# Optimization experiments

Hardware: AMD Instinct MI355X
Metric: run time of the kernel (lower is better)

Reference implementation:

```python
import jax, jax.numpy as jnp
import numpy as np

B, N = 32, 8192
NUM_CLASSES = 40
SA1_DIMS = (3, 64, 64, 128)      # grouped relative xyz only (in_channels=3 -> no extra features)
SA2_DIMS = (131, 128, 128, 256)  # 128 SA1 features + 3 relative xyz
LOC_DIMS = (256, 256, 512, 1024)
GLOB_DIMS = (1024, 512, 256)


def _fps(xyz, m):
    """Farthest point sampling. xyz: [B,N,3] -> indices [B,m] (first index is point 0)."""
    b, n, _ = xyz.shape
    big = jnp.asarray(1e10, xyz.dtype)

    def step(carry, _):
        dists, last = carry                                   # [B,N], [B]
        p = jnp.take_along_axis(xyz, last[:, None, None], axis=1)  # [B,1,3]
        d = jnp.sum((xyz - p) ** 2, axis=-1)                  # [B,N]
        dists = jnp.minimum(dists, d)
        nxt = jnp.argmax(dists, axis=-1).astype(jnp.int32)
        return (dists, nxt), nxt

    init = (jnp.full((b, n), big, xyz.dtype), jnp.zeros((b,), jnp.int32))
    _, rest = jax.lax.scan(step, init, None, length=m - 1)    # [m-1,B]
    return jnp.concatenate([jnp.zeros((b, 1), jnp.int32), rest.T], axis=1)


def _ball_query(xyz, new_xyz, radius, k):
    """First-k points within radius of each centroid, padded with the first hit (CUDA ball_query semantics)."""
    d2 = jnp.sum((new_xyz[:, :, None, :] - xyz[:, None, :, :]) ** 2, axis=-1)  # [B,M,N]
    valid = d2 < radius * radius
    n = xyz.shape[1]
    ar = jnp.arange(n, dtype=jnp.int32)
    order_key = jnp.where(valid, ar, ar + n)                  # valid points sort first, in index order
    _, idx = jax.lax.top_k(-order_key, k)                     # [B,M,K] first-k valid indices
    num_valid = jnp.sum(valid, axis=-1)                       # [B,M]
    idx = jnp.where(jnp.arange(k) < num_valid[..., None], idx, idx[..., :1])
    return idx.astype(jnp.int32)


_gather = jax.vmap(lambda p, i: p[i])  # p:[N,C], i:[M,K] -> [M,K,C], vmapped over batch


def _sa(xyz, feats, m, radius, k, ws, bs):
    """PointNetSAModule: FPS -> ball query -> group (relative xyz [+feat]) -> SharedMLP -> max over K."""
    cidx = _fps(xyz, m)
    new_xyz = jnp.take_along_axis(xyz, cidx[:, :, None], axis=1)   # [B,m,3]
    idx = _ball_query(xyz, new_xyz, radius, k)                     # [B,m,k]
    x = _gather(xyz, idx) - new_xyz[:, :, None, :]                 # [B,m,k,3]
    if feats is not None:
        x = jnp.concatenate([x, _gather(feats, idx)], axis=-1)
    for w, b in zip(ws, bs):  # Conv2d(1x1)+BN(eval, folded)+ReLU
        x = jax.nn.relu(jnp.einsum('bmkc,oc->bmko', x, w) + b)
    return new_xyz, jnp.max(x, axis=2)                             # [B,m,C_out]


def _forward(points, sa1_w0, sa1_b0, sa1_w1, sa1_b1, sa1_w2, sa1_b2,
             sa2_w0, sa2_b0, sa2_w1, sa2_b1, sa2_w2, sa2_b2,
             loc_w0, loc_b0, loc_w1, loc_b1, loc_w2, loc_b2,
             glob_w0, glob_b0, glob_w1, glob_b1, cls_w, cls_b):
    xyz = jnp.transpose(points, (0, 2, 1))                         # [B,N,3]
    new_xyz, feats = _sa(xyz, None, 512, 0.2, 32,
                         (sa1_w0, sa1_w1, sa1_w2), (sa1_b0, sa1_b1, sa1_b2))
    _, feats = _sa(new_xyz, feats, 128, 0.4, 64,
                   (sa2_w0, sa2_w1, sa2_w2), (sa2_b0, sa2_b1, sa2_b2))
    x = feats                                                      # [B,128,256]
    for w, b in ((loc_w0, loc_b0), (loc_w1, loc_b1), (loc_w2, loc_b2)):
        x = jax.nn.relu(jnp.einsum('bnc,oc->bno', x, w) + b)       # SharedMLP (Conv1d+BN+ReLU)
    x = jnp.max(x, axis=1)                                         # global max-pool -> [B,1024]
    for w, b in ((glob_w0, glob_b0), (glob_w1, glob_b1)):          # MLP (dropout in eval = identity)
        x = jax.nn.relu(x @ w.T + b)
    return x @ cls_w.T + cls_b                                     # cls_logits [B,40]


def setup_inputs() -> dict:
    key = jax.random.key(0)
    ks = iter(jax.random.split(key, 64))
    inp = {}
    # unit-cube point cloud so radii 0.2/0.4 are geometrically meaningful
    inp['points'] = jax.random.uniform(next(ks), (B, 3, N), jnp.float32, -1.0, 1.0)

    def lin(co, ci):
        return jax.random.normal(next(ks), (co, ci), jnp.float32) / np.sqrt(ci)

    for name, dims in (('sa1', SA1_DIMS), ('sa2', SA2_DIMS), ('loc', LOC_DIMS)):
        for i in range(len(dims) - 1):
            inp[f'{name}_w{i}'] = lin(dims[i + 1], dims[i])
            inp[f'{name}_b{i}'] = 0.01 * jax.random.normal(next(ks), (dims[i + 1],), jnp.float32)
    for i in range(2):
        inp[f'glob_w{i}'] = lin(GLOB_DIMS[i + 1], GLOB_DIMS[i])
        inp[f'glob_b{i}'] = 0.01 * jax.random.normal(next(ks), (GLOB_DIMS[i + 1],), jnp.float32)
    inp['cls_w'] = lin(NUM_CLASSES, GLOB_DIMS[-1])
    inp['cls_b'] = jnp.zeros((NUM_CLASSES,), jnp.float32)
    return inp


def reference(points, sa1_w0, sa1_b0, sa1_w1, sa1_b1, sa1_w2, sa1_b2,
              sa2_w0, sa2_b0, sa2_w1, sa2_b1, sa2_w2, sa2_b2,
              loc_w0, loc_b0, loc_w1, loc_b1, loc_w2, loc_b2,
              glob_w0, glob_b0, glob_w1, glob_b1, cls_w, cls_b):
    return _forward(points, sa1_w0, sa1_b0, sa1_w1, sa1_b1, sa1_w2, sa1_b2,
                    sa2_w0, sa2_b0, sa2_w1, sa2_b1, sa2_w2, sa2_b2,
                    loc_w0, loc_b0, loc_w1, loc_b1, loc_w2, loc_b2,
                    glob_w0, glob_b0, glob_w1, glob_b1, cls_w, cls_b)
```

## Files before the change

kernel.cpp:

```cpp
#include <hip/hip_runtime.h>
#include <hip/hip_bf16.h>
#include <cstdint>

#define CDIV(a,b) (((a)+(b)-1)/(b))

typedef short s8v __attribute__((ext_vector_type(8)));
typedef float f4v __attribute__((ext_vector_type(4)));
typedef float f2v __attribute__((ext_vector_type(2)));

__device__ __forceinline__ unsigned short f2bf_bits(float v) {
  __hip_bfloat16 b = __float2bfloat16(v);
  unsigned short u; __builtin_memcpy(&u, &b, 2);
  return u;
}
__device__ __forceinline__ void bsplit(float v, unsigned short& h, unsigned short& l) {
  __hip_bfloat16 hb = __float2bfloat16(v);
  float hf = __bfloat162float(hb);
  unsigned short hu; __builtin_memcpy(&hu, &hb, 2);
  h = hu;
  l = f2bf_bits(v - hf);
}

__device__ __forceinline__ void agpr_put(float& slot, float v) {
  asm volatile("v_accvgpr_write_b32 %0, %1" : "=a"(slot) : "v"(v));
}
__device__ __forceinline__ float agpr_get(const float& slot) {
  float v;
  asm volatile("v_accvgpr_read_b32 %0, %1" : "=v"(v) : "a"(slot));
  return v;
}

__device__ __forceinline__ f2v pk_add(f2v a, f2v b) {
  f2v d; asm("v_pk_add_f32 %0, %1, %2" : "=v"(d) : "v"(a), "v"(b)); return d;
}
__device__ __forceinline__ f2v pk_mul(f2v a, f2v b) {
  f2v d; asm("v_pk_mul_f32 %0, %1, %2" : "=v"(d) : "v"(a), "v"(b)); return d;
}
__device__ __forceinline__ f2v pk_fma(f2v a, f2v b, f2v c) {
  f2v d; asm("v_pk_fma_f32 %0, %1, %2, %3" : "=v"(d) : "v"(a), "v"(b), "v"(c)); return d;
}

template<int C>
__device__ __forceinline__ unsigned dpp32(unsigned v) {
  return (unsigned)__builtin_amdgcn_update_dpp((int)v, (int)v, C, 0xF, 0xF, false);
}
template<int C>
__device__ __forceinline__ unsigned long long red_key(unsigned long long pk) {
  unsigned lo = dpp32<C>((unsigned)pk);
  unsigned hi = dpp32<C>((unsigned)(pk >> 32));
  unsigned long long p2 = ((unsigned long long)hi << 32) | lo;
  return (p2 > pk) ? p2 : pk;
}

template<int NPTS, int MOUT, int NTHR>
__global__ __launch_bounds__(NTHR, 1) void fps_kernel(
    const float* __restrict__ pts, int bstride, int cstride,
    float* __restrict__ aos, float* __restrict__ soa)
{
  constexpr int PPT = NPTS / NTHR;
  constexpr int NP2 = PPT / 2;
  constexpr int NW  = NTHR / 64;
  const int b = blockIdx.x, t = threadIdx.x;
  const int lane = t & 63;
  const int wid = t >> 6;
  const float* px = pts + (size_t)b * bstride;
  const float* py = px + cstride;
  const float* pz = px + 2 * cstride;
  __shared__ float s_x[NPTS], s_y[NPTS], s_z[NPTS];
  __shared__ unsigned long long s_key[2][NW > 1 ? NW : 1];
  __shared__ int s_out[MOUT];

  float ax[PPT], ay[PPT], az[PPT];
  f2v dsv[NP2];
#pragma unroll
  for (int j = 0; j < PPT; ++j) {
    int i = t + j * NTHR;
    float x = px[i], y = py[i], z = pz[i];
    s_x[i] = x; s_y[i] = y; s_z[i] = z;
    agpr_put(ax[j], x); agpr_put(ay[j], y); agpr_put(az[j], z);
  }
#pragma unroll
  for (int q = 0; q < NP2; ++q) dsv[q] = (f2v){1e10f, 1e10f};
  if (t == 0) s_out[0] = 0;
  float lx = px[0], ly = py[0], lz = pz[0];
  __syncthreads();

  for (int it = 1; it < MOUT; ++it) {
    const f2v nlx = (f2v){-lx, -lx};
    const f2v nly = (f2v){-ly, -ly};
    const f2v nlz = (f2v){-lz, -lz};
    float bestv = -1.0f; int bestj = 0;
#pragma unroll
    for (int q = 0; q < NP2; ++q) {
      f2v x2, y2, z2;
      x2.x = agpr_get(ax[2 * q]); x2.y = agpr_get(ax[2 * q + 1]);
      y2.x = agpr_get(ay[2 * q]); y2.y = agpr_get(ay[2 * q + 1]);
      z2.x = agpr_get(az[2 * q]); z2.y = agpr_get(az[2 * q + 1]);
      f2v dx = pk_add(x2, nlx);
      f2v dy = pk_add(y2, nly);
      f2v dz = pk_add(z2, nlz);
      f2v d2 = pk_fma(dz, dz, pk_fma(dy, dy, pk_mul(dx, dx)));
      float nd0 = fminf(dsv[q].x, d2.x);
      float nd1 = fminf(dsv[q].y, d2.y);
      dsv[q].x = nd0; dsv[q].y = nd1;
      if (nd0 > bestv) { bestv = nd0; bestj = 2 * q; }
      if (nd1 > bestv) { bestv = nd1; bestj = 2 * q + 1; }
    }
    const int besti = t + bestj * NTHR;
    unsigned long long pk =
        ((unsigned long long)__float_as_uint(bestv) << 32) | (unsigned)(~(unsigned)besti);
    pk = red_key<0x111>(pk);
    pk = red_key<0x112>(pk);
    pk = red_key<0x114>(pk);
    pk = red_key<0x118>(pk);
    pk = red_key<0x142>(pk);
    pk = red_key<0x143>(pk);
    int widx;
    if constexpr (NW == 1) {
      widx = (int)(~(unsigned)__builtin_amdgcn_readlane((int)(unsigned)pk, 63));
    } else {
      const int pb = it & 1;
      if (lane == 63) s_key[pb][wid] = pk;
      __syncthreads();
      unsigned long long ck = s_key[pb][lane & (NW - 1)];
      if (NW >= 2)  ck = red_key<0x111>(ck);
      if (NW >= 4)  ck = red_key<0x112>(ck);
      if (NW >= 8)  ck = red_key<0x114>(ck);
      if (NW >= 16) ck = red_key<0x118>(ck);
      widx = (int)(~(unsigned)__builtin_amdgcn_readlane((int)(unsigned)ck, NW - 1));
    }
    lx = s_x[widx]; ly = s_y[widx]; lz = s_z[widx];
    if (t == 0) s_out[it] = widx;
  }
  __syncthreads();
  for (int i = t; i < MOUT; i += NTHR) {
    const int idx = s_out[i];
    const float x = s_x[idx], y = s_y[idx], z = s_z[idx];
    float* a = aos + ((size_t)b * MOUT + i) * 3;
    a[0] = x; a[1] = y; a[2] = z;
    soa[(size_t)b * 3 * MOUT + i]            = x;
    soa[(size_t)b * 3 * MOUT + MOUT + i]     = y;
    soa[(size_t)b * 3 * MOUT + 2 * MOUT + i] = z;
  }
}

template<int NPTS, int KNB, int MC>
__global__ __launch_bounds__(64) void ballq_wave(
    const float* __restrict__ pts, int bstride, int cstride,
    const float* __restrict__ cents, int* __restrict__ out, float r2)
{
  constexpr int NCH = NPTS / 128;
  const int g = blockIdx.x;
  const int b = g / MC;
  const int lane = threadIdx.x;
  const float* px = pts + (size_t)b * bstride;
  const float* py = px + cstride;
  const float* pz = px + 2 * cstride;
  const float cx = cents[g * 3 + 0], cy = cents[g * 3 + 1], cz = cents[g * 3 + 2];
  __shared__ int s_idx[KNB];
  float ax0 = px[lane],      ay0 = py[lane],      az0 = pz[lane];
  float ax1 = px[64 + lane], ay1 = py[64 + lane], az1 = pz[64 + lane];
  int base = 0;
  const unsigned long long below = (1ull << lane) - 1ull;
  for (int c = 0; c < NCH; ++c) {
    float X0 = ax0, Y0 = ay0, Z0 = az0;
    float X1 = ax1, Y1 = ay1, Z1 = az1;
    if (c + 1 < NCH) {
      int i0 = (c + 1) * 128 + lane;
      ax0 = px[i0];      ay0 = py[i0];      az0 = pz[i0];
      ax1 = px[i0 + 64]; ay1 = py[i0 + 64]; az1 = pz[i0 + 64];
    }
    float dx0 = X0 - cx, dy0 = Y0 - cy, dz0 = Z0 - cz;
    float dx1 = X1 - cx, dy1 = Y1 - cy, dz1 = Z1 - cz;
    bool v0 = (dx0 * dx0 + dy0 * dy0 + dz0 * dz0) < r2;
    bool v1 = (dx1 * dx1 + dy1 * dy1 + dz1 * dz1) < r2;
    unsigned long long m0 = __ballot(v0);
    unsigned long long m1 = __ballot(v1);
    int r0 = __popcll(m0 & below);
    int p0 = base + r0;
    if (v0 && p0 < KNB) s_idx[p0] = c * 128 + lane;
    int base1 = base + __popcll(m0);
    int r1 = __popcll(m1 & below);
    int p1 = base1 + r1;
    if (v1 && p1 < KNB) s_idx[p1] = c * 128 + 64 + lane;
    base = base1 + __popcll(m1);
    if (base >= KNB) break;
  }
  int total = base < KNB ? base : KNB;
  int first = s_idx[0];
  if (lane < KNB)
    out[(size_t)g * KNB + lane] = (lane < total) ? s_idx[lane] : first;
}

__device__ void fps2_embed(
    const float* __restrict__ soa_in, int b,
    float* __restrict__ aos, float* __restrict__ soa,
    float* fx, float* fy, float* fz, int* fout,
    unsigned long long* fkey , int t)
{
  const int lane = t & 63, wid = t >> 6;
  const float* px = soa_in + (size_t)b * 1536;
  const float* py = px + 512;
  const float* pz = px + 1024;
  float x0, y0, z0, x1, y1, z1;
  {
    const int i0 = t, i1 = t + 256;
    x0 = px[i0]; y0 = py[i0]; z0 = pz[i0];
    x1 = px[i1]; y1 = py[i1]; z1 = pz[i1];
    fx[i0] = x0; fy[i0] = y0; fz[i0] = z0;
    fx[i1] = x1; fy[i1] = y1; fz[i1] = z1;
  }
  f2v ds = (f2v){1e10f, 1e10f};
  if (t == 0) fout[0] = 0;
  float lx = px[0], ly = py[0], lz = pz[0];
  __syncthreads();
  for (int it = 1; it < 128; ++it) {
    f2v X = (f2v){x0, x1}, Y = (f2v){y0, y1}, Z = (f2v){z0, z1};
    f2v dx = pk_add(X, (f2v){-lx, -lx});
    f2v dy = pk_add(Y, (f2v){-ly, -ly});
    f2v dz = pk_add(Z, (f2v){-lz, -lz});
    f2v d2 = pk_fma(dz, dz, pk_fma(dy, dy, pk_mul(dx, dx)));
    float nd0 = fminf(ds.x, d2.x);
    float nd1 = fminf(ds.y, d2.y);
    ds.x = nd0; ds.y = nd1;
    float bestv = nd0; int bestj = 0;
    if (nd1 > bestv) { bestv = nd1; bestj = 1; }
    const int besti = t + bestj * 256;
    unsigned long long pk =
        ((unsigned long long)__float_as_uint(bestv) << 32) | (unsigned)(~(unsigned)besti);
    pk = red_key<0x111>(pk);
    pk = red_key<0x112>(pk);
    pk = red_key<0x114>(pk);
    pk = red_key<0x118>(pk);
    pk = red_key<0x142>(pk);
    pk = red_key<0x143>(pk);
    const int pb = it & 1;
    if (lane == 63) fkey[pb * 4 + wid] = pk;
    __syncthreads();
    unsigned long long ck = fkey[pb * 4 + (lane & 3)];
    ck = red_key<0x111>(ck);
    ck = red_key<0x112>(ck);
    const int widx = (int)(~(unsigned)__builtin_amdgcn_readlane((int)(unsigned)ck, 3));
    lx = fx[widx]; ly = fy[widx]; lz = fz[widx];
    if (t == 0) fout[it] = widx;
  }
  __syncthreads();
  if (t < 128) {
    const int idx = fout[t];
    const float x = fx[idx], y = fy[idx], z = fz[idx];
    float* a = aos + ((size_t)b * 128 + t) * 3;
    a[0] = x; a[1] = y; a[2] = z;
    soa[(size_t)b * 384 + t]       = x;
    soa[(size_t)b * 384 + 128 + t] = y;
    soa[(size_t)b * 384 + 256 + t] = z;
  }
}

__global__ __launch_bounds__(256, 1) void sa1_fused(
    const float* __restrict__ pts, const int* __restrict__ idx1,
    const float* __restrict__ cents,
    const float* __restrict__ w0, const float* __restrict__ b0,
    const unsigned short* __restrict__ w1h, const unsigned short* __restrict__ w1l,
    const float* __restrict__ b1,
    const unsigned short* __restrict__ w2h, const unsigned short* __restrict__ w2l,
    const float* __restrict__ b2,
    unsigned short* __restrict__ f1h, unsigned short* __restrict__ f1l,
    const float* __restrict__ nx1_soa, float* __restrict__ nx2_aos,
    float* __restrict__ nx2_soa)
{
  __shared__ __align__(16) unsigned short sY[2][128 * 72];
  __shared__ __align__(16) unsigned short sZ[2][128 * 72];
  __shared__ __align__(16) unsigned short sW[2][64 * 72];
  __shared__ float sw0[192];
  __shared__ float sb0[64];

  const int tid = threadIdx.x, lane = tid & 63, wid = tid >> 6;
  const int wm = wid & 1, wn = wid >> 1;
  const int mn15 = lane & 15, kgrp = lane >> 4;

  if (blockIdx.x < 32) {
    float* fx = (float*)&sY[0][0];
    float* fy = fx + 512;
    float* fz = fy + 512;
    int*   fout = (int*)(fz + 512);
    unsigned long long* fkey = (unsigned long long*)(fout + 128);
    fps2_embed(nx1_soa, blockIdx.x, nx2_aos, nx2_soa, fx, fy, fz, fout, fkey, tid);
    return;
  }
  const int bk = blockIdx.x - 32;

  if (tid < 192) sw0[tid] = w0[tid];
  else sb0[tid - 192] = b0[tid - 192];
  for (int gi = tid; gi < 1024; gi += 256) {
    const int pl = gi >> 9, idx = gi & 511;
    const int n = idx >> 3, k8 = idx & 7;
    const uint4 v = ((const uint4*)(pl ? w1l : w1h))[idx];
    *(uint4*)&sW[pl][n * 72 + k8 * 8] = v;
  }
  __syncthreads();

  {
    const int rl = tid >> 1, half = tid & 1;
    const int r = bk * 128 + rl;
    const int gl = r >> 5, j = r & 31, b = gl >> 9;
    const int i = idx1[(size_t)gl * 32 + j];
    const float* px = pts + (size_t)b * 24576;
    const float x = px[i]         - cents[gl * 3 + 0];
    const float y = px[8192 + i]  - cents[gl * 3 + 1];
    const float z = px[16384 + i] - cents[gl * 3 + 2];
    union { unsigned short us[32]; uint4 v[4]; } ph, pl4;
#pragma unroll
    for (int u = 0; u < 32; ++u) {
      const int o = half * 32 + u;
      float v = sw0[o * 3] * x + sw0[o * 3 + 1] * y + sw0[o * 3 + 2] * z + sb0[o];
      v = fmaxf(v, 0.f);
      bsplit(v, ph.us[u], pl4.us[u]);
    }
    const int base = rl * 72 + half * 32;
#pragma unroll
    for (int g = 0; g < 4; ++g) {
      *(uint4*)&sY[0][base + g * 8] = ph.v[g];
      *(uint4*)&sY[1][base + g * 8] = pl4.v[g];
    }
  }
  __syncthreads();

  {
    f4v acc[4][2];
#pragma unroll
    for (int a = 0; a < 4; ++a)
#pragma unroll
      for (int c = 0; c < 2; ++c) acc[a][c] = (f4v){0.f, 0.f, 0.f, 0.f};
#pragma unroll
    for (int kc = 0; kc < 2; ++kc) {
      const int k0 = kc * 32;
      s8v af[2][4], bf[2][2];
#pragma unroll
      for (int mt = 0; mt < 4; ++mt) {
        const int m = wm * 64 + mt * 16 + mn15;
        af[0][mt] = *(const s8v*)&sY[0][m * 72 + k0 + kgrp * 8];
        af[1][mt] = *(const s8v*)&sY[1][m * 72 + k0 + kgrp * 8];
      }
#pragma unroll
      for (int nt = 0; nt < 2; ++nt) {
        const int n = wn * 32 + nt * 16 + mn15;
        bf[0][nt] = *(const s8v*)&sW[0][n * 72 + k0 + kgrp * 8];
        bf[1][nt] = *(const s8v*)&sW[1][n * 72 + k0 + kgrp * 8];
      }
#pragma unroll
      for (int mt = 0; mt < 4; ++mt)
#pragma unroll
        for (int nt = 0; nt < 2; ++nt) {
          acc[mt][nt] = __builtin_amdgcn_mfma_f32_16x16x32_bf16(af[0][mt], bf[0][nt], acc[mt][nt], 0, 0, 0);
          acc[mt][nt] = __builtin_amdgcn_mfma_f32_16x16x32_bf16(af[0][mt], bf[1][nt], acc[mt][nt], 0, 0, 0);
          acc[mt][nt] = __builtin_amdgcn_mfma_f32_16x16x32_bf16(af[1][mt], bf[0][nt], acc[mt][nt], 0, 0, 0);
        }
    }
#pragma unroll
    for (int nt = 0; nt < 2; ++nt) {
      const int n = wn * 32 + nt * 16 + mn15;
      const float bv = b1[n];
#pragma unroll
      for (int mt = 0; mt < 4; ++mt)
#pragma unroll
        for (int r = 0; r < 4; ++r) {
          const int m = wm * 64 + mt * 16 + (lane >> 4) * 4 + r;
          float v = fmaxf(acc[mt][nt][r] + bv, 0.f);
          unsigned short h, l; bsplit(v, h, l);
          sZ[0][m * 72 + n] = h;
          sZ[1][m * 72 + n] = l;
        }
    }
  }
  __syncthreads();

  for (int gi = tid; gi < 2048; gi += 256) {
    const int pl = gi >> 10, idx = gi & 1023;
    const int n = idx >> 3, k8 = idx & 7;
    const uint4 v = ((const uint4*)(pl ? w2l : w2h))[idx];
    *(uint4*)&sY[pl][n * 72 + k8 * 8] = v;
  }
  __syncthreads();

  {
    f4v acc[4][4];
#pragma unroll
    for (int a = 0; a < 4; ++a)
#pragma unroll
      for (int c = 0; c < 4; ++c) acc[a][c] = (f4v){0.f, 0.f, 0.f, 0.f};
#pragma unroll
    for (int kc = 0; kc < 2; ++kc) {
      const int k0 = kc * 32;
      s8v af[2][4], bf[2][4];
#pragma unroll
      for (int mt = 0; mt < 4; ++mt) {
        const int m = wm * 64 + mt * 16 + mn15;
        af[0][mt] = *(const s8v*)&sZ[0][m * 72 + k0 + kgrp * 8];
        af[1][mt] = *(const s8v*)&sZ[1][m * 72 + k0 + kgrp * 8];
      }
#pragma unroll
      for (int nt = 0; nt < 4; ++nt) {
        const int n = wn * 64 + nt * 16 + mn15;
        bf[0][nt] = *(const s8v*)&sY[0][n * 72 + k0 + kgrp * 8];
        bf[1][nt] = *(const s8v*)&sY[1][n * 72 + k0 + kgrp * 8];
      }
#pragma unroll
      for (int mt = 0; mt < 4; ++mt)
#pragma unroll
        for (int nt = 0; nt < 4; ++nt) {
          acc[mt][nt] = __builtin_amdgcn_mfma_f32_16x16x32_bf16(af[0][mt], bf[0][nt], acc[mt][nt], 0, 0, 0);
          acc[mt][nt] = __builtin_amdgcn_mfma_f32_16x16x32_bf16(af[0][mt], bf[1][nt], acc[mt][nt], 0, 0, 0);
          acc[mt][nt] = __builtin_amdgcn_mfma_f32_16x16x32_bf16(af[1][mt], bf[0][nt], acc[mt][nt], 0, 0, 0);
        }
    }
#pragma unroll
    for (int gq = 0; gq < 2; ++gq)
#pragma unroll
      for (int nt = 0; nt < 4; ++nt) {
        const int n = wn * 64 + nt * 16 + mn15;
        float v = -1e30f;
#pragma unroll
        for (int mt = 2 * gq; mt < 2 * gq + 2; ++mt)
#pragma unroll
          for (int r = 0; r < 4; ++r) v = fmaxf(v, acc[mt][nt][r]);
        v = fmaxf(v + b2[n], 0.f);
        v = fmaxf(v, __shfl_xor(v, 16, 64));
        v = fmaxf(v, __shfl_xor(v, 32, 64));
        if (lane < 16) {
          const size_t row = (size_t)bk * 4 + wm * 2 + gq;
          unsigned short h, l; bsplit(v, h, l);
          f1h[row * 128 + n] = h;
          f1l[row * 128 + n] = l;
        }
      }
  }
}

__global__ __launch_bounds__(256, 1) void sa2_fused(
    const unsigned short* __restrict__ f1h, const unsigned short* __restrict__ f1l,
    const float* __restrict__ nx1_aos, const float* __restrict__ nx2_aos,
    const int* __restrict__ idx2,
    const unsigned short* __restrict__ w1h, const unsigned short* __restrict__ w1l,
    const float* __restrict__ b1,
    const unsigned short* __restrict__ w2h, const unsigned short* __restrict__ w2l,
    const float* __restrict__ b2,
    const unsigned short* __restrict__ w3h, const unsigned short* __restrict__ w3l,
    const float* __restrict__ b3,
    unsigned short* __restrict__ f2h, unsigned short* __restrict__ f2l)
{
  __shared__ __align__(16) unsigned short sX[2][64 * 160];
  __shared__ __align__(16) unsigned short sY[2][64 * 136];
  __shared__ __align__(16) unsigned short sW[4][2][32 * 40];

  const int tid = threadIdx.x, lane = tid & 63, wid = tid >> 6;
  const int mn15 = lane & 15, kgrp = lane >> 4;
  const int gg = blockIdx.x;
  const int bb = gg >> 7;

  {
    const int r = tid >> 2, q = tid & 3;
    const int i = idx2[(size_t)gg * 64 + r];
    const int p = bb * 512 + i;
#pragma unroll
    for (int pl = 0; pl < 2; ++pl) {
      const uint4* src = (const uint4*)((pl ? f1l : f1h) + (size_t)p * 128);
#pragma unroll
      for (int g = 0; g < 4; ++g)
        *(uint4*)&sX[pl][r * 160 + (q * 4 + g) * 8] = src[q * 4 + g];
    }
    if (q == 0) {
      union { unsigned short us[8]; uint4 v; } ph, pl4;
#pragma unroll
      for (int u = 0; u < 8; ++u) { ph.us[u] = 0; pl4.us[u] = 0; }
#pragma unroll
      for (int c = 0; c < 3; ++c) {
        float v = nx1_aos[(size_t)p * 3 + c] - nx2_aos[(size_t)gg * 3 + c];
        bsplit(v, ph.us[c], pl4.us[c]);
      }
      *(uint4*)&sX[0][r * 160 + 128] = ph.v;
      *(uint4*)&sX[1][r * 160 + 128] = pl4.v;
    } else {
      uint4 z = make_uint4(0, 0, 0, 0);
      *(uint4*)&sX[0][r * 160 + 128 + q * 8] = z;
      *(uint4*)&sX[1][r * 160 + 128 + q * 8] = z;
    }
  }
  __syncthreads();

  const int spl = lane >> 5, srow = lane & 31;
  unsigned short* swb = &sW[wid][0][0];

  {
    f4v acc[4][2];
#pragma unroll
    for (int a = 0; a < 4; ++a)
#pragma unroll
      for (int c = 0; c < 2; ++c) acc[a][c] = (f4v){0.f, 0.f, 0.f, 0.f};
    uint4 pf[4];
    {
      const unsigned short* s = (spl ? w1l : w1h) + (size_t)(wid * 32 + srow) * 160;
#pragma unroll
      for (int g = 0; g < 4; ++g) pf[g] = *(const uint4*)(s + g * 8);
    }
#pragma unroll
    for (int c = 0; c < 5; ++c) {
      unsigned short* d = swb + spl * 1280 + srow * 40;
#pragma unroll
      for (int g = 0; g < 4; ++g) *(uint4*)(d + g * 8) = pf[g];
      if (c < 4) {
        const unsigned short* s = (spl ? w1l : w1h) + (size_t)(wid * 32 + srow) * 160 + (c + 1) * 32;
#pragma unroll
        for (int g = 0; g < 4; ++g) pf[g] = *(const uint4*)(s + g * 8);
      }
      const int k0 = c * 32;
      s8v af[2][4], bf[2][2];
#pragma unroll
      for (int mt = 0; mt < 4; ++mt) {
        const int m = mt * 16 + mn15;
        af[0][mt] = *(const s8v*)&sX[0][m * 160 + k0 + kgrp * 8];
        af[1][mt] = *(const s8v*)&sX[1][m * 160 + k0 + kgrp * 8];
      }
#pragma unroll
      for (int nt = 0; nt < 2; ++nt) {
        const int nl = nt * 16 + mn15;
        bf[0][nt] = *(const s8v*)&swb[0 * 1280 + nl * 40 + kgrp * 8];
        bf[1][nt] = *(const s8v*)&swb[1 * 1280 + nl * 40 + kgrp * 8];
      }
#pragma unroll
      for (int mt = 0; mt < 4; ++mt)
#pragma unroll
        for (int nt = 0; nt < 2; ++nt) {
          acc[mt][nt] = __builtin_amdgcn_mfma_f32_16x16x32_bf16(af[0][mt], bf[0][nt], acc[mt][nt], 0, 0, 0);
          acc[mt][nt] = __builtin_amdgcn_mfma_f32_16x16x32_bf16(af[0][mt], bf[1][nt], acc[mt][nt], 0, 0, 0);
          acc[mt][nt] = __builtin_amdgcn_mfma_f32_16x16x32_bf16(af[1][mt], bf[0][nt], acc[mt][nt], 0, 0, 0);
        }
    }
#pragma unroll
    for (int nt = 0; nt < 2; ++nt) {
      const int n = wid * 32 + nt * 16 + mn15;
      const float bv = b1[n];
#pragma unroll
      for (int mt = 0; mt < 4; ++mt)
#pragma unroll
        for (int r = 0; r < 4; ++r) {
          const int m = mt * 16 + kgrp * 4 + r;
          float v = fmaxf(acc[mt][nt][r] + bv, 0.f);
          unsigned short h, l; bsplit(v, h, l);
          sY[0][m * 136 + n] = h;
          sY[1][m * 136 + n] = l;
        }
    }
  }
  __syncthreads();

  {
    f4v acc[4][2];
#pragma unroll
    for (int a = 0; a < 4; ++a)
#pragma unroll
      for (int c = 0; c < 2; ++c) acc[a][c] = (f4v){0.f, 0.f, 0.f, 0.f};
    uint4 pf[4];
    {
      const unsigned short* s = (spl ? w2l : w2h) + (size_t)(wid * 32 + srow) * 128;
#pragma unroll
      for (int g = 0; g < 4; ++g) pf[g] = *(const uint4*)(s + g * 8);
    }
#pragma unroll
    for (int c = 0; c < 4; ++c) {
      unsigned short* d = swb + spl * 1280 + srow * 40;
#pragma unroll
      for (int g = 0; g < 4; ++g) *(uint4*)(d + g * 8) = pf[g];
      if (c < 3) {
        const unsigned short* s = (spl ? w2l : w2h) + (size_t)(wid * 32 + srow) * 128 + (c + 1) * 32;
#pragma unroll
        for (int g = 0; g < 4; ++g) pf[g] = *(const uint4*)(s + g * 8);
      }
      const int k0 = c * 32;
      s8v af[2][4], bf[2][2];
#pragma unroll
      for (int mt = 0; mt < 4; ++mt) {
        const int m = mt * 16 + mn15;
        af[0][mt] = *(const s8v*)&sY[0][m * 136 + k0 + kgrp * 8];
        af[1][mt] = *(const s8v*)&sY[1][m * 136 + k0 + kgrp * 8];
      }
#pragma unroll
      for (int nt = 0; nt < 2; ++nt) {
        const int nl = nt * 16 + mn15;
        bf[0][nt] = *(const s8v*)&swb[0 * 1280 + nl * 40 + kgrp * 8];
        bf[1][nt] = *(const s8v*)&swb[1 * 1280 + nl * 40 + kgrp * 8];
      }
#pragma unroll
      for (int mt = 0; mt < 4; ++mt)
#pragma unroll
        for (int nt = 0; nt < 2; ++nt) {
          acc[mt][nt] = __builtin_amdgcn_mfma_f32_16x16x32_bf16(af[0][mt], bf[0][nt], acc[mt][nt], 0, 0, 0);
          acc[mt][nt] = __builtin_amdgcn_mfma_f32_16x16x32_bf16(af[0][mt], bf[1][nt], acc[mt][nt], 0, 0, 0);
          acc[mt][nt] = __builtin_amdgcn_mfma_f32_16x16x32_bf16(af[1][mt], bf[0][nt], acc[mt][nt], 0, 0, 0);
        }
    }
#pragma unroll
    for (int nt = 0; nt < 2; ++nt) {
      const int n = wid * 32 + nt * 16 + mn15;
      const float bv = b2[n];
#pragma unroll
      for (int mt = 0; mt < 4; ++mt)
#pragma unroll
        for (int r = 0; r < 4; ++r) {
          const int m = mt * 16 + kgrp * 4 + r;
          float v = fmaxf(acc[mt][nt][r] + bv, 0.f);
          unsigned short h, l; bsplit(v, h, l);
          sX[0][m * 136 + n] = h;
          sX[1][m * 136 + n] = l;
        }
    }
  }
  __syncthreads();

#pragma unroll
  for (int h = 0; h < 2; ++h) {
    f4v acc[4][2];
#pragma unroll
    for (int a = 0; a < 4; ++a)
#pragma unroll
      for (int c = 0; c < 2; ++c) acc[a][c] = (f4v){0.f, 0.f, 0.f, 0.f};
    const int nb = wid * 64 + h * 32;
    uint4 pf[4];
    {
      const unsigned short* s = (spl ? w3l : w3h) + (size_t)(nb + srow) * 128;
#pragma unroll
      for (int g = 0; g < 4; ++g) pf[g] = *(const uint4*)(s + g * 8);
    }
#pragma unroll
    for (int c = 0; c < 4; ++c) {
      unsigned short* d = swb + spl * 1280 + srow * 40;
#pragma unroll
      for (int g = 0; g < 4; ++g) *(uint4*)(d + g * 8) = pf[g];
      if (c < 3) {
        const unsigned short* s = (spl ? w3l : w3h) + (size_t)(nb + srow) * 128 + (c + 1) * 32;
#pragma unroll
        for (int g = 0; g < 4; ++g) pf[g] = *(const uint4*)(s + g * 8);
      }
      const int k0 = c * 32;
      s8v af[2][4], bf[2][2];
#pragma unroll
      for (int mt = 0; mt < 4; ++mt) {
        const int m = mt * 16 + mn15;
        af[0][mt] = *(const s8v*)&sX[0][m * 136 + k0 + kgrp * 8];
        af[1][mt] = *(const s8v*)&sX[1][m * 136 + k0 + kgrp * 8];
      }
#pragma unroll
      for (int nt = 0; nt < 2; ++nt) {
        const int nl = nt * 16 + mn15;
        bf[0][nt] = *(const s8v*)&swb[0 * 1280 + nl * 40 + kgrp * 8];
        bf[1][nt] = *(const s8v*)&swb[1 * 1280 + nl * 40 + kgrp * 8];
      }
#pragma unroll
      for (int mt = 0; mt < 4; ++mt)
#pragma unroll
        for (int nt = 0; nt < 2; ++nt) {
          acc[mt][nt] = __builtin_amdgcn_mfma_f32_16x16x32_bf16(af[0][mt], bf[0][nt], acc[mt][nt], 0, 0, 0);
          acc[mt][nt] = __builtin_amdgcn_mfma_f32_16x16x32_bf16(af[0][mt], bf[1][nt], acc[mt][nt], 0, 0, 0);
          acc[mt][nt] = __builtin_amdgcn_mfma_f32_16x16x32_bf16(af[1][mt], bf[0][nt], acc[mt][nt], 0, 0, 0);
        }
    }
#pragma unroll
    for (int nt = 0; nt < 2; ++nt) {
      const int n = nb + nt * 16 + mn15;
      float v = -1e30f;
#pragma unroll
      for (int mt = 0; mt < 4; ++mt)
#pragma unroll
        for (int r = 0; r < 4; ++r) v = fmaxf(v, acc[mt][nt][r]);
      v = fmaxf(v + b3[n], 0.f);
      v = fmaxf(v, __shfl_xor(v, 16, 64));
      v = fmaxf(v, __shfl_xor(v, 32, 64));
      if (lane < 16) {
        unsigned short hh, ll; bsplit(v, hh, ll);
        f2h[(size_t)gg * 256 + n] = hh;
        f2l[(size_t)gg * 256 + n] = ll;
      }
    }
  }
}

struct WSplitArgs {
  const float* src[9];
  unsigned short* h[9];
  unsigned short* l[9];
  int K[9];
  int KP[9];
  int perm[9];
  int cum[10];
};
__global__ void wsplit_all(WSplitArgs a) {
  int i = blockIdx.x * 256 + threadIdx.x;
  if (i >= a.cum[9]) return;
  int s = 0;
#pragma unroll
  for (int t = 1; t < 9; ++t) s += (i >= a.cum[t]);
  int local = i - a.cum[s];
  int KP = a.KP[s], K = a.K[s];
  int r = local / KP, k = local - r * KP;
  int oc;
  if (a.perm[s]) oc = (k < 128) ? k + 3 : (k < 131 ? k - 128 : -1);
  else           oc = (k < K) ? k : -1;
  float v = (oc >= 0) ? a.src[s][(size_t)r * K + oc] : 0.f;
  unsigned short hb, lb; bsplit(v, hb, lb);
  a.h[s][local] = hb; a.l[s][local] = lb;
}

__device__ __forceinline__ void gl2lds16(const void* g, void* l, int lane) {
#if __has_builtin(__builtin_amdgcn_global_load_lds)
  __builtin_amdgcn_global_load_lds(
      (const __attribute__((address_space(1))) unsigned int*)g,
      (__attribute__((address_space(3))) unsigned int*)l, 16, 0, 0);
#else
  ((uint4*)l)[lane] = *(const uint4*)g;
#endif
}

template<int BN, int POOL>
__global__ __launch_bounds__(256, 1) void mfma_gemm(
    const unsigned short* __restrict__ Ah, const unsigned short* __restrict__ Al,
    const unsigned short* __restrict__ Wh, const unsigned short* __restrict__ Wl,
    const float* __restrict__ bias,
    unsigned short* __restrict__ Ch, unsigned short* __restrict__ Cl,
    float* __restrict__ Cf,
    int Kdim, int Ndim)
{
  constexpr int WTN = BN / 2, NT = WTN / 16;
  __shared__ unsigned short sA[2][128 * 32];
  __shared__ unsigned short sW[2][BN * 32];
  __shared__ float sPool[4][WTN];
  const int tid = threadIdx.x, lane = tid & 63, wid = tid >> 6;
  const int wm = wid & 1, wn = wid >> 1;
  const size_t bm0 = (size_t)blockIdx.y * 128;
  const int bn0 = blockIdx.x * BN;
  const int mn15 = lane & 15, kgrp = lane >> 4;

  f4v acc[4][NT];
#pragma unroll
  for (int a = 0; a < 4; ++a)
#pragma unroll
    for (int b = 0; b < NT; ++b) acc[a][b] = (f4v){0.f, 0.f, 0.f, 0.f};

  const int sc = lane & 3, srl = lane >> 2;

  for (int k0 = 0; k0 < Kdim; k0 += 32) {
#pragma unroll
    for (int hh = 0; hh < 2; ++hh) {
      const int R = wid * 32 + hh * 16;
      const int m = R + srl;
      const int kg = (sc - m - (m >> 2)) & 3;
      const size_t go = (bm0 + m) * (size_t)Kdim + k0 + kg * 8;
      gl2lds16(Ah + go, &sA[0][R * 32], lane);
      gl2lds16(Al + go, &sA[1][R * 32], lane);
    }
#pragma unroll
    for (int hh = 0; hh < 2; ++hh) {
      const int R = wid * 32 + hh * 16;
      const int n = R + srl;
      const int kg = (sc - n - (n >> 2)) & 3;
      const size_t go = (size_t)(bn0 + n) * Kdim + k0 + kg * 8;
      gl2lds16(Wh + go, &sW[0][R * 32], lane);
      gl2lds16(Wl + go, &sW[1][R * 32], lane);
    }
    __syncthreads();

    s8v af[2][4], bfr[2][NT];
#pragma unroll
    for (int mt = 0; mt < 4; ++mt) {
      const int m = wm * 64 + mt * 16 + mn15;
      const int cc = (kgrp + m + (m >> 2)) & 3;
      af[0][mt] = *(const s8v*)&sA[0][m * 32 + cc * 8];
      af[1][mt] = *(const s8v*)&sA[1][m * 32 + cc * 8];
    }
#pragma unroll
    for (int nt = 0; nt < NT; ++nt) {
      const int n = wn * WTN + nt * 16 + mn15;
      const int cc = (kgrp + n + (n >> 2)) & 3;
      bfr[0][nt] = *(const s8v*)&sW[0][n * 32 + cc * 8];
      bfr[1][nt] = *(const s8v*)&sW[1][n * 32 + cc * 8];
    }
#pragma unroll
    for (int mt = 0; mt < 4; ++mt)
#pragma unroll
      for (int nt = 0; nt < NT; ++nt) {
        acc[mt][nt] = __builtin_amdgcn_mfma_f32_16x16x32_bf16(af[0][mt], bfr[0][nt], acc[mt][nt], 0, 0, 0);
        acc[mt][nt] = __builtin_amdgcn_mfma_f32_16x16x32_bf16(af[0][mt], bfr[1][nt], acc[mt][nt], 0, 0, 0);
        acc[mt][nt] = __builtin_amdgcn_mfma_f32_16x16x32_bf16(af[1][mt], bfr[0][nt], acc[mt][nt], 0, 0, 0);
      }
    __syncthreads();
  }

  float bv[NT];
#pragma unroll
  for (int nt = 0; nt < NT; ++nt) bv[nt] = bias[bn0 + wn * WTN + nt * 16 + mn15];

  if (POOL == 0) {
#pragma unroll
    for (int mt = 0; mt < 4; ++mt)
#pragma unroll
      for (int nt = 0; nt < NT; ++nt) {
        const int n = bn0 + wn * WTN + nt * 16 + mn15;
#pragma unroll
        for (int r = 0; r < 4; ++r) {
          const size_t m = bm0 + wm * 64 + mt * 16 + (lane >> 4) * 4 + r;
          float v = fmaxf(acc[mt][nt][r] + bv[nt], 0.f);
          unsigned short h, l; bsplit(v, h, l);
          Ch[m * Ndim + n] = h;
          Cl[m * Ndim + n] = l;
        }
      }
  } else {
    float part[NT];
#pragma unroll
    for (int nt = 0; nt < NT; ++nt) {
      float v = -1e30f;
#pragma unroll
      for (int mt = 0; mt < 4; ++mt)
#pragma unroll
        for (int r = 0; r < 4; ++r) v = fmaxf(v, acc[mt][nt][r]);
      v = fmaxf(v + bv[nt], 0.f);
      v = fmaxf(v, __shfl_xor(v, 16, 64));
      v = fmaxf(v, __shfl_xor(v, 32, 64));
      part[nt] = v;
      if (lane < 16) sPool[wid][nt * 16 + mn15] = v;
    }
    __syncthreads();
    if (wm == 0 && lane < 16) {
#pragma unroll
      for (int nt = 0; nt < NT; ++nt) {
        float v = fmaxf(part[nt], sPool[wid + 1][nt * 16 + mn15]);
        const int n = bn0 + wn * WTN + nt * 16 + mn15;
        if (Cf) Cf[(size_t)(bm0 / 128) * Ndim + n] = v;
      }
    }
  }
}

__global__ __launch_bounds__(256) void head_kernel(
    const float* __restrict__ pooled,
    const float* __restrict__ w0, const float* __restrict__ b0,
    const float* __restrict__ w1, const float* __restrict__ b1,
    const float* __restrict__ wc, const float* __restrict__ bc,
    float* __restrict__ out)
{
  __shared__ float sx[1024];
  __shared__ float sy[512];
  __shared__ float sz[256];
  const int b = blockIdx.x, t = threadIdx.x;
  for (int i = t; i < 1024; i += 256) sx[i] = pooled[(size_t)b * 1024 + i];
  __syncthreads();
  for (int o = t; o < 512; o += 256) {
    const float4* w4 = (const float4*)(w0 + (size_t)o * 1024);
    const float4* x4 = (const float4*)sx;
    float acc = 0.f;
#pragma unroll 4
    for (int k = 0; k < 256; ++k) {
      float4 w = w4[k], x = x4[k];
      acc += w.x * x.x + w.y * x.y + w.z * x.z + w.w * x.w;
    }
    sy[o] = fmaxf(acc + b0[o], 0.f);
  }
  __syncthreads();
  if (t < 256) {
    const float4* w4 = (const float4*)(w1 + (size_t)t * 512);
    const float4* y4 = (const float4*)sy;
    float acc = 0.f;
#pragma unroll 4
    for (int k = 0; k < 128; ++k) {
      float4 w = w4[k], y = y4[k];
      acc += w.x * y.x + w.y * y.y + w.z * y.z + w.w * y.w;
    }
    sz[t] = fmaxf(acc + b1[t], 0.f);
  }
  __syncthreads();
  if (t < 40) {
    const float4* w4 = (const float4*)(wc + (size_t)t * 256);
    const float4* z4 = (const float4*)sz;
    float acc = 0.f;
#pragma unroll 4
    for (int k = 0; k < 64; ++k) {
      float4 w = w4[k], z = z4[k];
      acc += w.x * z.x + w.y * z.y + w.z * z.z + w.w * z.w;
    }
    out[(size_t)b * 40 + t] = acc + bc[t];
  }
}

extern "C" void kernel_launch(void* const* d_in, const int* in_sizes, int n_in,
                              void* d_out, int out_size, void* d_ws, size_t ws_size,
                              hipStream_t stream)
{
  (void)in_sizes; (void)n_in; (void)out_size; (void)ws_size;

  const float* points  = (const float*)d_in[0];
  const float* sa1_w[3] = {(const float*)d_in[1], (const float*)d_in[3], (const float*)d_in[5]};
  const float* sa1_b[3] = {(const float*)d_in[2], (const float*)d_in[4], (const float*)d_in[6]};
  const float* sa2_w[3] = {(const float*)d_in[7], (const float*)d_in[9], (const float*)d_in[11]};
  const float* sa2_b[3] = {(const float*)d_in[8], (const float*)d_in[10], (const float*)d_in[12]};
  const float* loc_w[3] = {(const float*)d_in[13], (const float*)d_in[15], (const float*)d_in[17]};
  const float* loc_b[3] = {(const float*)d_in[14], (const float*)d_in[16], (const float*)d_in[18]};
  const float* glob_w0 = (const float*)d_in[19];
  const float* glob_b0 = (const float*)d_in[20];
  const float* glob_w1 = (const float*)d_in[21];
  const float* glob_b1 = (const float*)d_in[22];
  const float* cls_w   = (const float*)d_in[23];
  const float* cls_b   = (const float*)d_in[24];

  char* base = (char*)d_ws;
  size_t off = 0;
  auto alloc = [&](size_t nbytes) -> void* {
    void* p = base + off;
    off += (nbytes + 255) & ~(size_t)255;
    return p;
  };

  const size_t XE = (size_t)4096 * 512;
  const size_t YE = (size_t)4096 * 256;
  unsigned short* Xh = (unsigned short*)alloc(XE * 2);
  unsigned short* Xl = (unsigned short*)alloc(XE * 2);
  unsigned short* Yh = (unsigned short*)alloc(YE * 2);
  unsigned short* Yl = (unsigned short*)alloc(YE * 2);
  unsigned short* f1h = (unsigned short*)alloc((size_t)16384 * 128 * 2);
  unsigned short* f1l = (unsigned short*)alloc((size_t)16384 * 128 * 2);
  unsigned short* f2h = (unsigned short*)alloc((size_t)4096 * 256 * 2);
  unsigned short* f2l = (unsigned short*)alloc((size_t)4096 * 256 * 2);

  const int  wrows[9] = {64, 64, 128, 128, 128, 256, 256, 512, 1024};
  const int  wK[9]    = {3, 64, 64, 131, 128, 128, 256, 256, 512};
  const int  wKP[9]   = {32, 64, 64, 160, 128, 128, 256, 256, 512};
  const float* wsrc[9] = {sa1_w[0], sa1_w[1], sa1_w[2],
                          sa2_w[0], sa2_w[1], sa2_w[2],
                          loc_w[0], loc_w[1], loc_w[2]};
  unsigned short *wph[9], *wpl[9];
  WSplitArgs wa;
  int cum = 0;
  for (int s = 0; s < 9; ++s) {
    size_t e = (size_t)wrows[s] * wKP[s];
    wph[s] = (unsigned short*)alloc(e * 2);
    wpl[s] = (unsigned short*)alloc(e * 2);
    wa.src[s] = wsrc[s]; wa.h[s] = wph[s]; wa.l[s] = wpl[s];
    wa.K[s] = wK[s]; wa.KP[s] = wKP[s]; wa.cum[s] = cum;
    wa.perm[s] = (s == 3) ? 1 : 0;
    cum += wrows[s] * wKP[s];
  }
  wa.cum[9] = cum;

  float* nx1_aos = (float*)alloc((size_t)32 * 512 * 3 * 4);
  float* nx1_soa = (float*)alloc((size_t)32 * 512 * 3 * 4);
  int*   idx1    = (int*)  alloc((size_t)32 * 512 * 32 * 4);
  float* nx2_aos = (float*)alloc((size_t)32 * 128 * 3 * 4);
  float* nx2_soa = (float*)alloc((size_t)32 * 128 * 3 * 4);
  int*   idx2    = (int*)  alloc((size_t)32 * 128 * 64 * 4);
  float* pooled  = (float*)alloc((size_t)32 * 1024 * 4);

  const float r2a = (float)(0.2 * 0.2);
  const float r2b = (float)(0.4 * 0.4);

  wsplit_all<<<CDIV(cum, 256), 256, 0, stream>>>(wa);

  fps_kernel<8192, 512, 512><<<32, 512, 0, stream>>>(points, 24576, 8192, nx1_aos, nx1_soa);
  ballq_wave<8192, 32, 512><<<32 * 512, 64, 0, stream>>>(points, 24576, 8192, nx1_aos, idx1, r2a);

  sa1_fused<<<32 + 4096, 256, 0, stream>>>(
      points, idx1, nx1_aos, sa1_w[0], sa1_b[0],
      wph[1], wpl[1], sa1_b[1], wph[2], wpl[2], sa1_b[2], f1h, f1l,
      nx1_soa, nx2_aos, nx2_soa);

  ballq_wave<512, 64, 128><<<32 * 128, 64, 0, stream>>>(nx1_soa, 1536, 512, nx2_aos, idx2, r2b);

  sa2_fused<<<4096, 256, 0, stream>>>(
      f1h, f1l, nx1_aos, nx2_aos, idx2,
      wph[3], wpl[3], sa2_b[0],
      wph[4], wpl[4], sa2_b[1],
      wph[5], wpl[5], sa2_b[2],
      f2h, f2l);

  mfma_gemm<128, 0><<<dim3(2, 32), 256, 0, stream>>>(
      f2h, f2l, wph[6], wpl[6], loc_b[0], Yh, Yl, nullptr, 256, 256);
  mfma_gemm<128, 0><<<dim3(4, 32), 256, 0, stream>>>(
      Yh, Yl, wph[7], wpl[7], loc_b[1], Xh, Xl, nullptr, 256, 512);
  mfma_gemm<128, 128><<<dim3(8, 32), 256, 0, stream>>>(
      Xh, Xl, wph[8], wpl[8], loc_b[2], nullptr, nullptr, pooled, 512, 1024);

  head_kernel<<<32, 256, 0, stream>>>(pooled, glob_w0, glob_b0,
                                      glob_w1, glob_b1, cls_w, cls_b, (float*)d_out);
}
```

Baseline: 1.157 ms.

## Fuse ball queries into SA1 and SA2 kernels, dropping global index buffers

The two standalone ball-query kernels are removed. Their neighbour search now runs per wave inside sa1_fused (one centroid per wave, four per block) and in wave 0 of sa2_fused. Neighbour indices stay in shared memory instead of going through global idx1/idx2 buffers. This cuts two launches and the index write/read traffic. In exchange, the search loop runs inside kernels bounded to one block per SIMD and loses its load prefetch, so memory latency may be less hidden.

```diff
diff --git a/kernel.cpp b/kernel.cpp
--- a/kernel.cpp
+++ b/kernel.cpp
@@ -142,54 +142,6 @@
     soa[(size_t)b * 3 * MOUT + MOUT + i]     = y;
     soa[(size_t)b * 3 * MOUT + 2 * MOUT + i] = z;
   }
-}
-
-template<int NPTS, int KNB, int MC>
-__global__ __launch_bounds__(64) void ballq_wave(
-    const float* __restrict__ pts, int bstride, int cstride,
-    const float* __restrict__ cents, int* __restrict__ out, float r2)
-{
-  constexpr int NCH = NPTS / 128;
-  const int g = blockIdx.x;
-  const int b = g / MC;
-  const int lane = threadIdx.x;
-  const float* px = pts + (size_t)b * bstride;
-  const float* py = px + cstride;
-  const float* pz = px + 2 * cstride;
-  const float cx = cents[g * 3 + 0], cy = cents[g * 3 + 1], cz = cents[g * 3 + 2];
-  __shared__ int s_idx[KNB];
-  float ax0 = px[lane],      ay0 = py[lane],      az0 = pz[lane];
-  float ax1 = px[64 + lane], ay1 = py[64 + lane], az1 = pz[64 + lane];
-  int base = 0;
-  const unsigned long long below = (1ull << lane) - 1ull;
-  for (int c = 0; c < NCH; ++c) {
-    float X0 = ax0, Y0 = ay0, Z0 = az0;
-    float X1 = ax1, Y1 = ay1, Z1 = az1;
-    if (c + 1 < NCH) {
-      int i0 = (c + 1) * 128 + lane;
-      ax0 = px[i0];      ay0 = py[i0];      az0 = pz[i0];
-      ax1 = px[i0 + 64]; ay1 = py[i0 + 64]; az1 = pz[i0 + 64];
-    }
-    float dx0 = X0 - cx, dy0 = Y0 - cy, dz0 = Z0 - cz;
-    float dx1 = X1 - cx, dy1 = Y1 - cy, dz1 = Z1 - cz;
-    bool v0 = (dx0 * dx0 + dy0 * dy0 + dz0 * dz0) < r2;
-    bool v1 = (dx1 * dx1 + dy1 * dy1 + dz1 * dz1) < r2;
-    unsigned long long m0 = __ballot(v0);
-    unsigned long long m1 = __ballot(v1);
-    int r0 = __popcll(m0 & below);
-    int p0 = base + r0;
-    if (v0 && p0 < KNB) s_idx[p0] = c * 128 + lane;
-    int base1 = base + __popcll(m0);
-    int r1 = __popcll(m1 & below);
-    int p1 = base1 + r1;
-    if (v1 && p1 < KNB) s_idx[p1] = c * 128 + 64 + lane;
-    base = base1 + __popcll(m1);
-    if (base >= KNB) break;
-  }
-  int total = base < KNB ? base : KNB;
-  int first = s_idx[0];
-  if (lane < KNB)
-    out[(size_t)g * KNB + lane] = (lane < total) ? s_idx[lane] : first;
 }
 
 __device__ void fps2_embed(
@@ -257,7 +209,7 @@
 }
 
 __global__ __launch_bounds__(256, 1) void sa1_fused(
-    const float* __restrict__ pts, const int* __restrict__ idx1,
+    const float* __restrict__ pts,
     const float* __restrict__ cents,
     const float* __restrict__ w0, const float* __restrict__ b0,
     const unsigned short* __restrict__ w1h, const unsigned short* __restrict__ w1l,
@@ -266,13 +218,14 @@
     const float* __restrict__ b2,
     unsigned short* __restrict__ f1h, unsigned short* __restrict__ f1l,
     const float* __restrict__ nx1_soa, float* __restrict__ nx2_aos,
-    float* __restrict__ nx2_soa)
+    float* __restrict__ nx2_soa, float r2)
 {
   __shared__ __align__(16) unsigned short sY[2][128 * 72];
   __shared__ __align__(16) unsigned short sZ[2][128 * 72];
   __shared__ __align__(16) unsigned short sW[2][64 * 72];
   __shared__ float sw0[192];
   __shared__ float sb0[64];
+  __shared__ int s_idx1[4][32];
 
   const int tid = threadIdx.x, lane = tid & 63, wid = tid >> 6;
   const int wm = wid & 1, wn = wid >> 1;
@@ -289,6 +242,38 @@
   }
   const int bk = blockIdx.x - 32;
 
+  {
+    const int g = bk * 4 + wid;
+    const int b = g >> 9;
+    const float* px = pts + (size_t)b * 24576;
+    const float* py = px + 8192;
+    const float* pz = px + 16384;
+    const float cx = cents[g * 3 + 0], cy = cents[g * 3 + 1], cz = cents[g * 3 + 2];
+    const unsigned long long below = (1ull << lane) - 1ull;
+    int base = 0;
+    for (int c = 0; c < 64; ++c) {
+      const int i0 = c * 128 + lane;
+      float X0 = px[i0],      Y0 = py[i0],      Z0 = pz[i0];
+      float X1 = px[i0 + 64], Y1 = py[i0 + 64], Z1 = pz[i0 + 64];
+      float dx0 = X0 - cx, dy0 = Y0 - cy, dz0 = Z0 - cz;
+      float dx1 = X1 - cx, dy1 = Y1 - cy, dz1 = Z1 - cz;
+      bool v0 = (dx0 * dx0 + dy0 * dy0 + dz0 * dz0) < r2;
+      bool v1 = (dx1 * dx1 + dy1 * dy1 + dz1 * dz1) < r2;
+      unsigned long long m0 = __ballot(v0);
+      unsigned long long m1 = __ballot(v1);
+      int p0 = base + __popcll(m0 & below);
+      if (v0 && p0 < 32) s_idx1[wid][p0] = i0;
+      int base1 = base + __popcll(m0);
+      int p1 = base1 + __popcll(m1 & below);
+      if (v1 && p1 < 32) s_idx1[wid][p1] = i0 + 64;
+      base = base1 + __popcll(m1);
+      if (base >= 32) break;
+    }
+    int total = base < 32 ? base : 32;
+    int first = s_idx1[wid][0];
+    if (lane < 32 && lane >= total) s_idx1[wid][lane] = first;
+  }
+
   if (tid < 192) sw0[tid] = w0[tid];
   else sb0[tid - 192] = b0[tid - 192];
   for (int gi = tid; gi < 1024; gi += 256) {
@@ -301,9 +286,9 @@
 
   {
     const int rl = tid >> 1, half = tid & 1;
-    const int r = bk * 128 + rl;
-    const int gl = r >> 5, j = r & 31, b = gl >> 9;
-    const int i = idx1[(size_t)gl * 32 + j];
+    const int lgl = rl >> 5, j = rl & 31;
+    const int gl = bk * 4 + lgl, b = gl >> 9;
+    const int i = s_idx1[lgl][j];
     const float* px = pts + (size_t)b * 24576;
     const float x = px[i]         - cents[gl * 3 + 0];
     const float y = px[8192 + i]  - cents[gl * 3 + 1];
@@ -438,28 +423,60 @@
 
 __global__ __launch_bounds__(256, 1) void sa2_fused(
     const unsigned short* __restrict__ f1h, const unsigned short* __restrict__ f1l,
-    const float* __restrict__ nx1_aos, const float* __restrict__ nx2_aos,
-    const int* __restrict__ idx2,
+    const float* __restrict__ nx1_aos, const float* __restrict__ nx1_soa,
+    const float* __restrict__ nx2_aos,
     const unsigned short* __restrict__ w1h, const unsigned short* __restrict__ w1l,
     const float* __restrict__ b1,
     const unsigned short* __restrict__ w2h, const unsigned short* __restrict__ w2l,
     const float* __restrict__ b2,
     const unsigned short* __restrict__ w3h, const unsigned short* __restrict__ w3l,
     const float* __restrict__ b3,
-    unsigned short* __restrict__ f2h, unsigned short* __restrict__ f2l)
+    unsigned short* __restrict__ f2h, unsigned short* __restrict__ f2l, float r2)
 {
   __shared__ __align__(16) unsigned short sX[2][64 * 160];
   __shared__ __align__(16) unsigned short sY[2][64 * 136];
   __shared__ __align__(16) unsigned short sW[4][2][32 * 40];
+  __shared__ int s_idx2[64];
 
   const int tid = threadIdx.x, lane = tid & 63, wid = tid >> 6;
   const int mn15 = lane & 15, kgrp = lane >> 4;
   const int gg = blockIdx.x;
   const int bb = gg >> 7;
 
+  if (wid == 0) {
+    const float* px = nx1_soa + (size_t)bb * 1536;
+    const float* py = px + 512;
+    const float* pz = px + 1024;
+    const float cx = nx2_aos[gg * 3 + 0], cy = nx2_aos[gg * 3 + 1], cz = nx2_aos[gg * 3 + 2];
+    const unsigned long long below = (1ull << lane) - 1ull;
+    int base = 0;
+    for (int c = 0; c < 4; ++c) {
+      const int i0 = c * 128 + lane;
+      float X0 = px[i0],      Y0 = py[i0],      Z0 = pz[i0];
+      float X1 = px[i0 + 64], Y1 = py[i0 + 64], Z1 = pz[i0 + 64];
+      float dx0 = X0 - cx, dy0 = Y0 - cy, dz0 = Z0 - cz;
+      float dx1 = X1 - cx, dy1 = Y1 - cy, dz1 = Z1 - cz;
+      bool v0 = (dx0 * dx0 + dy0 * dy0 + dz0 * dz0) < r2;
+      bool v1 = (dx1 * dx1 + dy1 * dy1 + dz1 * dz1) < r2;
+      unsigned long long m0 = __ballot(v0);
+      unsigned long long m1 = __ballot(v1);
+      int p0 = base + __popcll(m0 & below);
+      if (v0 && p0 < 64) s_idx2[p0] = i0;
+      int base1 = base + __popcll(m0);
+      int p1 = base1 + __popcll(m1 & below);
+      if (v1 && p1 < 64) s_idx2[p1] = i0 + 64;
+      base = base1 + __popcll(m1);
+      if (base >= 64) break;
+    }
+    int total = base < 64 ? base : 64;
+    int first = s_idx2[0];
+    if (lane >= total) s_idx2[lane] = first;
+  }
+  __syncthreads();
+
   {
     const int r = tid >> 2, q = tid & 3;
-    const int i = idx2[(size_t)gg * 64 + r];
+    const int i = s_idx2[r];
     const int p = bb * 512 + i;
 #pragma unroll
     for (int pl = 0; pl < 2; ++pl) {
@@ -950,10 +967,8 @@
 
   float* nx1_aos = (float*)alloc((size_t)32 * 512 * 3 * 4);
   float* nx1_soa = (float*)alloc((size_t)32 * 512 * 3 * 4);
-  int*   idx1    = (int*)  alloc((size_t)32 * 512 * 32 * 4);
   float* nx2_aos = (float*)alloc((size_t)32 * 128 * 3 * 4);
   float* nx2_soa = (float*)alloc((size_t)32 * 128 * 3 * 4);
-  int*   idx2    = (int*)  alloc((size_t)32 * 128 * 64 * 4);
   float* pooled  = (float*)alloc((size_t)32 * 1024 * 4);
 
   const float r2a = (float)(0.2 * 0.2);
@@ -962,21 +977,18 @@
   wsplit_all<<<CDIV(cum, 256), 256, 0, stream>>>(wa);
 
   fps_kernel<8192, 512, 512><<<32, 512, 0, stream>>>(points, 24576, 8192, nx1_aos, nx1_soa);
-  ballq_wave<8192, 32, 512><<<32 * 512, 64, 0, stream>>>(points, 24576, 8192, nx1_aos, idx1, r2a);
 
   sa1_fused<<<32 + 4096, 256, 0, stream>>>(
-      points, idx1, nx1_aos, sa1_w[0], sa1_b[0],
+      points, nx1_aos, sa1_w[0], sa1_b[0],
       wph[1], wpl[1], sa1_b[1], wph[2], wpl[2], sa1_b[2], f1h, f1l,
-      nx1_soa, nx2_aos, nx2_soa);
-
-  ballq_wave<512, 64, 128><<<32 * 128, 64, 0, stream>>>(nx1_soa, 1536, 512, nx2_aos, idx2, r2b);
+      nx1_soa, nx2_aos, nx2_soa, r2a);
 
   sa2_fused<<<4096, 256, 0, stream>>>(
-      f1h, f1l, nx1_aos, nx2_aos, idx2,
+      f1h, f1l, nx1_aos, nx1_soa, nx2_aos,
       wph[3], wpl[3], sa2_b[0],
       wph[4], wpl[4], sa2_b[1],
       wph[5], wpl[5], sa2_b[2],
-      f2h, f2l);
+      f2h, f2l, r2b);
 
   mfma_gemm<128, 0><<<dim3(2, 32), 256, 0, stream>>>(
       f2h, f2l, wph[6], wpl[6], loc_b[0], Yh, Yl, nullptr, 256, 256);
```

Result: slower. 1.499 ms (+29.5%).
